# Kernel optimization log

Hardware: AMD Instinct MI355X
Metric: run time of the kernel (lower is better)

The kernel has to match this reference:

```python
import jax, jax.numpy as jnp
import numpy as np

B, T, D, H = 4, 2048, 1024, 16
HD = D // H


def setup_inputs() -> dict:
    key = jax.random.key(0)
    ks = jax.random.split(key, 6)
    s = 0.02
    return {
        "x": jax.random.normal(ks[0], (B, T, D), dtype=jnp.float32),
        "padding_mask": jnp.zeros((B, T), dtype=bool),
        "Wq": jax.random.normal(ks[1], (D, D), dtype=jnp.float32) * s,
        "Wk": jax.random.normal(ks[2], (D, D), dtype=jnp.float32) * s,
        "Wv": jax.random.normal(ks[3], (D, D), dtype=jnp.float32) * s,
        "Wo": jax.random.normal(ks[4], (D, D), dtype=jnp.float32) * s,
        "bo": jax.random.normal(ks[5], (D,), dtype=jnp.float32) * s,
    }


def reference(x, padding_mask, Wq, Wk, Wv, Wo, bo):
    # torch nn.Linear: y = x @ W.T
    b, t, d = x.shape
    q = (x @ Wq.T).reshape(b, t, H, HD).transpose(0, 2, 1, 3)  # [B,H,T,hd]
    k = (x @ Wk.T).reshape(b, t, H, HD).transpose(0, 2, 1, 3)
    v = (x @ Wv.T).reshape(b, t, H, HD).transpose(0, 2, 1, 3)

    scores = jnp.einsum("bhid,bhjd->bhij", q, k) / jnp.sqrt(jnp.float32(HD))
    causal = jnp.tril(jnp.ones((t, t), dtype=bool))  # [T,T]
    neg_inf = jnp.float32(-jnp.inf)
    scores = jnp.where(causal[None, None, :, :], scores, neg_inf)
    scores = jnp.where(padding_mask[:, None, None, :], neg_inf, scores)

    attn = jax.nn.softmax(scores, axis=-1)
    out = jnp.einsum("bhij,bhjd->bhid", attn, v)
    out = out.transpose(0, 2, 1, 3).reshape(b, t, d)
    out = out @ Wo.T + bo
    nonpad = (~padding_mask)[:, :, None].astype(out.dtype)
    return out * nonpad
```

## Files before the change

### kernel.cpp

```cpp
#include <hip/hip_runtime.h>

#define B_ 4
#define T_ 2048
#define D_ 1024
#define H_ 16
#define BT_ (B_ * T_)
#define QSCALE (0.125f * 1.44269504088896f)

typedef unsigned short u16;
typedef __attribute__((ext_vector_type(8))) __bf16 bf16x8;
typedef __attribute__((ext_vector_type(4))) float f32x4;

__device__ __forceinline__ u16 f2bf(float f) {
  unsigned u = __builtin_bit_cast(unsigned, f);
  u += 0x7FFFu + ((u >> 16) & 1u);
  return (u16)(u >> 16);
}

__device__ __forceinline__ void gload16(const void* g, void* l) {
  __builtin_amdgcn_global_load_lds(
      (const __attribute__((address_space(1))) void*)g,
      (__attribute__((address_space(3))) void*)l, 16, 0, 0);
}

__global__ void cvt_bf16(const float* __restrict__ in, u16* __restrict__ out, int n4) {
  int i = blockIdx.x * 256 + threadIdx.x;
  if (i >= n4) return;
  const float4 v = ((const float4*)in)[i];
  ushort4 o;
  o.x = f2bf(v.x); o.y = f2bf(v.y); o.z = f2bf(v.z); o.w = f2bf(v.w);
  ((ushort4*)out)[i] = o;
}

__global__ void cvt_wts(const float* __restrict__ Wq, const float* __restrict__ Wk,
                        const float* __restrict__ Wv, const float* __restrict__ Wo,
                        u16* __restrict__ wdst,
                        const unsigned char* __restrict__ pm, unsigned char* __restrict__ fl) {
  const int by = blockIdx.y;
  if (by < 4) {
    const float* src = (by == 0) ? Wq : (by == 1) ? Wk : (by == 2) ? Wv : Wo;
    const int i = blockIdx.x * 256 + threadIdx.x;
    const float4 v = ((const float4*)src)[i];
    ushort4 o;
    o.x = f2bf(v.x); o.y = f2bf(v.y); o.z = f2bf(v.z); o.w = f2bf(v.w);
    ((ushort4*)(wdst + (size_t)by * D_ * D_))[i] = o;
  } else if (blockIdx.x == 0 && threadIdx.x < 128) {
    const int i = threadIdx.x;
    const unsigned long long* p = (const unsigned long long*)(pm + i * 64);
    unsigned long long acc = 0;
#pragma unroll
    for (int k = 0; k < 8; ++k) acc |= p[k];
    fl[i] = acc ? 1 : 0;
  }
}

template<int MODE>
__global__ __launch_bounds__(256, 2) void gemm_bt(
    const u16* __restrict__ A, const u16* __restrict__ Bw,
    float* __restrict__ Cf, const float* __restrict__ bias,
    const unsigned char* __restrict__ rowmask,
    u16* __restrict__ Cq, u16* __restrict__ Ck, u16* __restrict__ Cvt)
{
  __shared__ __align__(16) u16 sA[128 * 64];
  __shared__ __align__(16) u16 sB[128 * 64];
  const int tid = threadIdx.x;
  const int lane = tid & 63, wave = tid >> 6;
  const int g = lane >> 4, s15 = lane & 15;
  const int bm = blockIdx.x * 128, bn = blockIdx.y * 128;
  const int wr = wave >> 1, wc = wave & 1;

  const int srow = lane >> 3;
  const int scol = ((lane & 7) ^ srow) << 3;

  f32x4 acc[4][4] = {};

  for (int kt = 0; kt < 16; ++kt) {
    __syncthreads();
    const int k0 = kt << 6;
#pragma unroll
    for (int c = 0; c < 4; ++c) {
      const int chunk = c * 4 + wave;
      gload16(A  + (size_t)(bm + chunk * 8 + srow) * 1024 + k0 + scol, (char*)sA + chunk * 1024);
      gload16(Bw + (size_t)(bn + chunk * 8 + srow) * 1024 + k0 + scol, (char*)sB + chunk * 1024);
    }
    __syncthreads();
#pragma unroll
    for (int kk = 0; kk < 2; ++kk) {
      const int cb = ((kk << 6) | (g << 4)) ^ ((s15 & 7) << 4);
      bf16x8 af[4], bf[4];
#pragma unroll
      for (int mm = 0; mm < 4; ++mm)
        af[mm] = *(const bf16x8*)((const char*)sA + (wr * 64 + mm * 16 + s15) * 128 + cb);
#pragma unroll
      for (int nn = 0; nn < 4; ++nn)
        bf[nn] = *(const bf16x8*)((const char*)sB + (wc * 64 + nn * 16 + s15) * 128 + cb);
#pragma unroll
      for (int mm = 0; mm < 4; ++mm)
#pragma unroll
        for (int nn = 0; nn < 4; ++nn)
          acc[mm][nn] = __builtin_amdgcn_mfma_f32_16x16x32_bf16(af[mm], bf[nn], acc[mm][nn], 0, 0, 0);
    }
  }

  if (MODE == 1) {
    const int region = bn >> 10;
    const float a = (region == 0) ? QSCALE : 1.f;
#pragma unroll
    for (int mm = 0; mm < 4; ++mm)
#pragma unroll
      for (int nn = 0; nn < 4; ++nn) {
        const int col = bn + wc * 64 + nn * 16 + s15;
        const int colr = col & 1023;
        const int row0 = bm + wr * 64 + mm * 16 + (g << 2);
        if (region == 2) {
          ushort4 w;
          w.x = f2bf(acc[mm][nn][0]); w.y = f2bf(acc[mm][nn][1]);
          w.z = f2bf(acc[mm][nn][2]); w.w = f2bf(acc[mm][nn][3]);
          *(ushort4*)(Cvt + (size_t)colr * BT_ + row0) = w;
        } else {
          u16* dst = region ? Ck : Cq;
#pragma unroll
          for (int r = 0; r < 4; ++r)
            dst[(size_t)(row0 + r) * 1024 + colr] = f2bf(acc[mm][nn][r] * a);
        }
      }
  } else {
#pragma unroll
    for (int mm = 0; mm < 4; ++mm)
#pragma unroll
      for (int nn = 0; nn < 4; ++nn) {
        const int col = bn + wc * 64 + nn * 16 + s15;
        const int row0 = bm + wr * 64 + mm * 16 + (g << 2);
        const float bv = bias[col];
#pragma unroll
        for (int r = 0; r < 4; ++r) {
          float v = acc[mm][nn][r] + bv;
          v = rowmask[row0 + r] ? 0.f : v;
          Cf[(size_t)(row0 + r) * 1024 + col] = v;
        }
      }
  }
}

__global__ __launch_bounds__(512, 4) void attn_fwd(
    const u16* __restrict__ Q, const u16* __restrict__ K,
    const u16* __restrict__ VT, const unsigned char* __restrict__ pm,
    const unsigned char* __restrict__ tileflag, u16* __restrict__ O)
{
  __shared__ __align__(16) u16 sK[2][64 * 64];
  __shared__ __align__(16) u16 sV[2][64 * 64];
  const int tid = threadIdx.x;
  const int lane = tid & 63, wave = tid >> 6;
  const int g = lane >> 4, s15 = lane & 15;
  const int bh = blockIdx.x, b = bh >> 4, h = bh & 15;
  const int j = blockIdx.y;
  const size_t tokbase = (size_t)b * T_;

  const int qw0 = j * 128 + wave * 16;
  const int qw1 = (15 - j) * 128 + wave * 16;
  const int nt = 32 - 2 * j;

  const int srow = tid >> 3;
  const int sc = (tid & 7) ^ (srow & 7);
  const u16* Kb0 = K + tokbase * D_ + h * 64 + sc * 8;
  const u16* Vb0 = VT + (size_t)(h * 64) * BT_ + tokbase + sc * 8;

  bf16x8 qf[2][2];
#pragma unroll
  for (int ks = 0; ks < 2; ++ks) {
    qf[0][ks] = *(const bf16x8*)(Q + (tokbase + qw0 + s15) * D_ + h * 64 + ks * 32 + g * 8);
    qf[1][ks] = *(const bf16x8*)(Q + (tokbase + qw1 + s15) * D_ + h * 64 + ks * 32 + g * 8);
  }

  f32x4 o[2][4] = {};
  f32x4 l4[2] = {};

  gload16(Kb0 + (size_t)srow * D_,  (char*)(&sK[0][0]) + tid * 16);
  gload16(Vb0 + (size_t)srow * BT_, (char*)(&sV[0][0]) + tid * 16);
  __syncthreads();

  for (int t = 0; t < nt; ++t) {
    const int kv0 = t << 6;
    if (t + 1 < nt) {
      const int nb = (t + 1) & 1;
      gload16(Kb0 + (size_t)(kv0 + 64 + srow) * D_,  (char*)(&sK[nb][0]) + tid * 16);
      gload16(Vb0 + (size_t)srow * BT_ + kv0 + 64,   (char*)(&sV[nb][0]) + tid * 16);
    }

    const bool act0 = (kv0 <= qw0 + 15);
    const bool act1 = (kv0 <= qw1 + 15);
    const u16* kb_ = &sK[t & 1][0];
    const u16* vb_ = &sV[t & 1][0];

    f32x4 st[4][2] = {};
#pragma unroll
    for (int ks = 0; ks < 2; ++ks) {
      bf16x8 kf[4];
#pragma unroll
      for (int jf = 0; jf < 4; ++jf)
        kf[jf] = *(const bf16x8*)(kb_ + (jf * 16 + s15) * 64 + (((ks * 4 + g) ^ (s15 & 7)) << 3));
      __builtin_amdgcn_s_setprio(1);
      if (act0)
#pragma unroll
        for (int jf = 0; jf < 4; ++jf)
          st[jf][0] = __builtin_amdgcn_mfma_f32_16x16x32_bf16(kf[jf], qf[0][ks], st[jf][0], 0, 0, 0);
      if (act1)
#pragma unroll
        for (int jf = 0; jf < 4; ++jf)
          st[jf][1] = __builtin_amdgcn_mfma_f32_16x16x32_bf16(kf[jf], qf[1][ks], st[jf][1], 0, 0, 0);
      __builtin_amdgcn_s_setprio(0);
    }

    if (act0 && kv0 + 63 > qw0) {
      const int iq = qw0 + s15;
#pragma unroll
      for (int jf = 0; jf < 4; ++jf) {
        const int jb = kv0 + jf * 16 + g * 4;
#pragma unroll
        for (int r = 0; r < 4; ++r)
          if (jb + r > iq) st[jf][0][r] = -1e30f;
      }
    }
    if (act1 && kv0 + 63 > qw1) {
      const int iq = qw1 + s15;
#pragma unroll
      for (int jf = 0; jf < 4; ++jf) {
        const int jb = kv0 + jf * 16 + g * 4;
#pragma unroll
        for (int r = 0; r < 4; ++r)
          if (jb + r > iq) st[jf][1][r] = -1e30f;
      }
    }
    if (tileflag[b * 32 + t]) {
#pragma unroll
      for (int jf = 0; jf < 4; ++jf) {
        const int jb = kv0 + jf * 16 + g * 4;
        uchar4 p4 = *(const uchar4*)(pm + b * T_ + jb);
        const unsigned char* pr = (const unsigned char*)&p4;
#pragma unroll
        for (int r = 0; r < 4; ++r)
          if (pr[r]) { st[jf][0][r] = -1e30f; st[jf][1][r] = -1e30f; }
      }
    }

    if (act0)
#pragma unroll
      for (int jf = 0; jf < 4; ++jf) {
#pragma unroll
        for (int r = 0; r < 4; ++r)
          st[jf][0][r] = __builtin_amdgcn_exp2f(st[jf][0][r]);
        l4[0] += st[jf][0];
      }
    if (act1)
#pragma unroll
      for (int jf = 0; jf < 4; ++jf) {
#pragma unroll
        for (int r = 0; r < 4; ++r)
          st[jf][1][r] = __builtin_amdgcn_exp2f(st[jf][1][r]);
        l4[1] += st[jf][1];
      }

#pragma unroll
    for (int kb2 = 0; kb2 < 2; ++kb2) {
      bf16x8 vf[4];
#pragma unroll
      for (int df = 0; df < 4; ++df)
        vf[df] = *(const bf16x8*)(vb_ + (df * 16 + s15) * 64 + (((kb2 * 4 + g) ^ (s15 & 7)) << 3));
#pragma unroll
      for (int nf = 0; nf < 2; ++nf) {
        if (nf == 0 ? !act0 : !act1) continue;
        unsigned w00, w01, w10, w11;
        asm("v_cvt_pk_bf16_f32 %0, %1, %2" : "=v"(w00) : "v"(st[2*kb2][nf][0]),   "v"(st[2*kb2][nf][1]));
        asm("v_cvt_pk_bf16_f32 %0, %1, %2" : "=v"(w01) : "v"(st[2*kb2][nf][2]),   "v"(st[2*kb2][nf][3]));
        asm("v_cvt_pk_bf16_f32 %0, %1, %2" : "=v"(w10) : "v"(st[2*kb2+1][nf][0]), "v"(st[2*kb2+1][nf][1]));
        asm("v_cvt_pk_bf16_f32 %0, %1, %2" : "=v"(w11) : "v"(st[2*kb2+1][nf][2]), "v"(st[2*kb2+1][nf][3]));
        asm("v_permlane32_swap_b32 %0, %1" : "+v"(w00), "+v"(w10));
        asm("v_permlane16_swap_b32 %0, %1" : "+v"(w00), "+v"(w10));
        asm("v_permlane32_swap_b32 %0, %1" : "+v"(w01), "+v"(w11));
        asm("v_permlane16_swap_b32 %0, %1" : "+v"(w01), "+v"(w11));
        union { unsigned u[4]; bf16x8 v; } pf;
        pf.u[0] = w00; pf.u[1] = w01; pf.u[2] = w10; pf.u[3] = w11;
        __builtin_amdgcn_s_setprio(1);
#pragma unroll
        for (int df = 0; df < 4; ++df)
          o[nf][df] = __builtin_amdgcn_mfma_f32_16x16x32_bf16(vf[df], pf.v, o[nf][df], 0, 0, 0);
        __builtin_amdgcn_s_setprio(0);
      }
    }
    __syncthreads();
  }

#pragma unroll
  for (int nf = 0; nf < 2; ++nf) {
    float lv = (l4[nf][0] + l4[nf][1]) + (l4[nf][2] + l4[nf][3]);
    lv += __shfl_xor(lv, 16);
    lv += __shfl_xor(lv, 32);
    const float inv = 1.f / lv;
    const int qw = nf ? qw1 : qw0;
    u16* orow = O + (tokbase + qw + s15) * D_ + h * 64 + g * 4;
#pragma unroll
    for (int df = 0; df < 4; ++df) {
      ushort4 w;
      w.x = f2bf(o[nf][df][0] * inv); w.y = f2bf(o[nf][df][1] * inv);
      w.z = f2bf(o[nf][df][2] * inv); w.w = f2bf(o[nf][df][3] * inv);
      *(ushort4*)(orow + df * 16) = w;
    }
  }
}

extern "C" void kernel_launch(void* const* d_in, const int* in_sizes, int n_in,
                              void* d_out, int out_size, void* d_ws, size_t ws_size,
                              hipStream_t stream)
{
  const float* x  = (const float*)d_in[0];
  const unsigned char* pm = (const unsigned char*)d_in[1];
  const float* Wq = (const float*)d_in[2];
  const float* Wk = (const float*)d_in[3];
  const float* Wv = (const float*)d_in[4];
  const float* Wo = (const float*)d_in[5];
  const float* bo = (const float*)d_in[6];
  float* out = (float*)d_out;

  char* w = (char*)d_ws;
  u16* xb  = (u16*)w; w += (size_t)BT_ * D_ * 2;
  u16* wqb = (u16*)w; w += (size_t)D_ * D_ * 2;
  u16* wkb = (u16*)w; w += (size_t)D_ * D_ * 2;
  u16* wvb = (u16*)w; w += (size_t)D_ * D_ * 2;
  u16* wob = (u16*)w; w += (size_t)D_ * D_ * 2;
  u16* qb  = (u16*)w; w += (size_t)BT_ * D_ * 2;
  u16* kbf = (u16*)w; w += (size_t)BT_ * D_ * 2;
  u16* vt  = (u16*)w; w += (size_t)BT_ * D_ * 2;
  u16* ao  = (u16*)w; w += (size_t)BT_ * D_ * 2;
  unsigned char* flags = (unsigned char*)w; w += 256;
  (void)wkb; (void)wvb;

  const int nx4 = BT_ * D_ / 4;
  cvt_bf16<<<nx4 / 256, 256, 0, stream>>>(x, xb, nx4);
  cvt_wts<<<dim3(1024, 5), 256, 0, stream>>>(Wq, Wk, Wv, Wo, wqb, pm, flags);

  gemm_bt<1><<<dim3(64, 24), 256, 0, stream>>>(xb, wqb, nullptr, nullptr, nullptr, qb, kbf, vt);

  attn_fwd<<<dim3(B_ * H_, 8), 512, 0, stream>>>(qb, kbf, vt, pm, flags, ao);

  gemm_bt<0><<<dim3(64, 8), 256, 0, stream>>>(ao, wob, out, bo, pm, nullptr, nullptr, nullptr);
}
```

Baseline: 143.9 us.

## Triple-buffer K/V tiles in attention with partial vmcnt waits

```diff
diff --git a/kernel.cpp b/kernel.cpp
--- a/kernel.cpp
+++ b/kernel.cpp
@@ -8,6 +8,7 @@
 #define QSCALE (0.125f * 1.44269504088896f)
 
 typedef unsigned short u16;
+typedef unsigned long long u64;
 typedef __attribute__((ext_vector_type(8))) __bf16 bf16x8;
 typedef __attribute__((ext_vector_type(4))) float f32x4;
 
@@ -147,8 +148,8 @@
     const u16* __restrict__ VT, const unsigned char* __restrict__ pm,
     const unsigned char* __restrict__ tileflag, u16* __restrict__ O)
 {
-  __shared__ __align__(16) u16 sK[2][64 * 64];
-  __shared__ __align__(16) u16 sV[2][64 * 64];
+  __shared__ __align__(16) u16 sK[3][64 * 64];
+  __shared__ __align__(16) u16 sV[3][64 * 64];
   const int tid = threadIdx.x;
   const int lane = tid & 63, wave = tid >> 6;
   const int g = lane >> 4, s15 = lane & 15;
@@ -165,6 +166,10 @@
   const u16* Kb0 = K + tokbase * D_ + h * 64 + sc * 8;
   const u16* Vb0 = VT + (size_t)(h * 64) * BT_ + tokbase + sc * 8;
 
+  u64 flq[4];
+#pragma unroll
+  for (int q = 0; q < 4; ++q) flq[q] = ((const u64*)(tileflag + b * 32))[q];
+
   bf16x8 qf[2][2];
 #pragma unroll
   for (int ks = 0; ks < 2; ++ks) {
@@ -175,22 +180,26 @@
   f32x4 o[2][4] = {};
   f32x4 l4[2] = {};
 
-  gload16(Kb0 + (size_t)srow * D_,  (char*)(&sK[0][0]) + tid * 16);
-  gload16(Vb0 + (size_t)srow * BT_, (char*)(&sV[0][0]) + tid * 16);
-  __syncthreads();
-
+  gload16(Kb0 + (size_t)srow * D_,        (char*)(&sK[0][0]) + tid * 16);
+  gload16(Vb0 + (size_t)srow * BT_,       (char*)(&sV[0][0]) + tid * 16);
+  gload16(Kb0 + (size_t)(64 + srow) * D_, (char*)(&sK[1][0]) + tid * 16);
+  gload16(Vb0 + (size_t)srow * BT_ + 64,  (char*)(&sV[1][0]) + tid * 16);
+  asm volatile("s_waitcnt vmcnt(2) lgkmcnt(0)" ::: "memory");
+  __builtin_amdgcn_s_barrier();
+  asm volatile("" ::: "memory");
+
+  int rd = 0, st2 = 2;
   for (int t = 0; t < nt; ++t) {
     const int kv0 = t << 6;
-    if (t + 1 < nt) {
-      const int nb = (t + 1) & 1;
-      gload16(Kb0 + (size_t)(kv0 + 64 + srow) * D_,  (char*)(&sK[nb][0]) + tid * 16);
-      gload16(Vb0 + (size_t)srow * BT_ + kv0 + 64,   (char*)(&sV[nb][0]) + tid * 16);
+    if (t + 2 < nt) {
+      gload16(Kb0 + (size_t)(kv0 + 128 + srow) * D_, (char*)(&sK[st2][0]) + tid * 16);
+      gload16(Vb0 + (size_t)srow * BT_ + kv0 + 128,  (char*)(&sV[st2][0]) + tid * 16);
     }
 
     const bool act0 = (kv0 <= qw0 + 15);
     const bool act1 = (kv0 <= qw1 + 15);
-    const u16* kb_ = &sK[t & 1][0];
-    const u16* vb_ = &sV[t & 1][0];
+    const u16* kb_ = &sK[rd][0];
+    const u16* vb_ = &sV[rd][0];
 
     f32x4 st[4][2] = {};
 #pragma unroll
@@ -231,7 +240,7 @@
           if (jb + r > iq) st[jf][1][r] = -1e30f;
       }
     }
-    if (tileflag[b * 32 + t]) {
+    if ((flq[t >> 3] >> ((t & 7) * 8)) & 0xff) {
 #pragma unroll
       for (int jf = 0; jf < 4; ++jf) {
         const int jb = kv0 + jf * 16 + g * 4;
@@ -287,7 +296,15 @@
         __builtin_amdgcn_s_setprio(0);
       }
     }
-    __syncthreads();
+
+    if (t + 1 < nt) {
+      if (t + 2 < nt) asm volatile("s_waitcnt vmcnt(2) lgkmcnt(0)" ::: "memory");
+      else            asm volatile("s_waitcnt vmcnt(0) lgkmcnt(0)" ::: "memory");
+      __builtin_amdgcn_s_barrier();
+      asm volatile("" ::: "memory");
+    }
+    rd  = (rd  == 2) ? 0 : rd + 1;
+    st2 = (st2 == 2) ? 0 : st2 + 1;
   }
 
 #pragma unroll
```

Result: no change. 142.1 us, median of 2 (-1.3%).
